# Kernel optimization log

Measured on AMD Instinct MI355X. Metric: run time of the kernel, lower is better.

## Reference

```python
import jax, jax.numpy as jnp
import numpy as np

B, IN, H, OUT = 1024, 512, 1024, 512   # tokens, input, hidden (MoE width), output
E, K, LAYERS = 8, 2, 10                 # experts, top-k, repeated MoE applications
EPS = 1e-10
LOSS_COEF = 0.01


def setup_inputs() -> dict:
    key = jax.random.key(0)
    ks = jax.random.split(key, 8)
    s = 0.02  # small init scale for weights
    return {
        "x": jax.random.normal(ks[0], (B, IN), jnp.float32),
        "enc_w": jax.random.normal(ks[1], (IN, H), jnp.float32) * s,
        "enc_b": jnp.zeros((H,), jnp.float32),
        "w_gate": jax.random.normal(ks[2], (H, E), jnp.float32) * s,
        "w1": jax.random.normal(ks[3], (E, H, H), jnp.float32) * s,
        "b1": jnp.zeros((E, H), jnp.float32),
        "w2": jax.random.normal(ks[4], (E, H, H), jnp.float32) * s,
        "b2": jnp.zeros((E, H), jnp.float32),
        "dec_w": jax.random.normal(ks[5], (H, OUT), jnp.float32) * s,
        "dec_b": jnp.zeros((OUT,), jnp.float32),
    }


def _cv_squared(v):
    # torch .var() is unbiased (ddof=1)
    return jnp.var(v, ddof=1) / (jnp.mean(v) ** 2 + EPS)


def _moe_layer(h, w_gate, w1, b1, w2, b2):
    # top-k gating (eval / no-noise path of noisy_top_k_gating)
    logits = h @ w_gate                                  # [B, E]
    top_vals, top_idx = jax.lax.top_k(logits, K)         # [B, K]
    gk = jax.nn.softmax(top_vals, axis=-1)               # softmax over top-k logits
    b = h.shape[0]
    gates = jnp.zeros((b, E), h.dtype).at[jnp.arange(b)[:, None], top_idx].set(gk)
    importance = gates.sum(axis=0)                       # [E]
    load = (gates > 0).sum(axis=0).astype(h.dtype)       # [E]
    aux = LOSS_COEF * (_cv_squared(importance) + _cv_squared(load))
    # experts: Linear -> ReLU -> Linear; combine weighted by gates
    # (dense-over-experts form; math identical to sparse dispatch/combine)
    hid = jax.nn.relu(jnp.einsum('bh,ehf->bef', h, w1) + b1)  # [B, E, H]
    y = jnp.einsum('bef,efo->beo', hid, w2) + b2              # [B, E, H]
    out = jnp.einsum('be,beo->bo', gates, y)                  # [B, H]
    return out, aux


def reference(x, enc_w, enc_b, w_gate, w1, b1, w2, b2, dec_w, dec_b):
    h = jax.nn.relu(x @ enc_w + enc_b)
    loss = jnp.zeros((), h.dtype)
    for _ in range(LAYERS):  # same MoE module (shared params) applied 10 times
        h, aux = _moe_layer(h, w_gate, w1, b1, w2, b2)
        loss = loss + aux
    out = jax.nn.relu(h @ dec_w + dec_b)
    return out, loss
```

## Files before the change

kernel.cpp:

```cpp
#include <hip/hip_runtime.h>
#include <math.h>

#define TPB 256
#define GTPB 512
typedef unsigned short u16;
typedef unsigned int u32;
typedef __bf16 bf16x8 __attribute__((ext_vector_type(8)));
typedef float f32x4 __attribute__((ext_vector_type(4)));

namespace {
constexpr int NTOK  = 1024;
constexpr int IND   = 512;
constexpr int HD    = 1024;
constexpr int OUTD  = 512;
constexpr int NE    = 8;
constexpr int NSLOT = 2048;
}

__device__ __forceinline__ u16 f2bf(float f) {
  u32 x = __float_as_uint(f);
  x += 0x7fffu + ((x >> 16) & 1u);
  return (u16)(x >> 16);
}
__device__ __forceinline__ float bf2f(u16 u) { return __uint_as_float(((u32)u) << 16); }
__device__ __forceinline__ void split2(float v, u16& h, u16& l) {
  h = f2bf(v);
  l = f2bf(v - bf2f(h));
}

__device__ __forceinline__ void gll16(const void* g, void* l) {
  __builtin_amdgcn_global_load_lds((const __attribute__((address_space(1))) void*)g,
                                   (__attribute__((address_space(3))) void*)l, 16, 0, 0);
}


__global__ __launch_bounds__(TPB)
void transpose_split(const float* __restrict__ in, u16* __restrict__ ohi,
                     u16* __restrict__ olo, int K, int N)
{
  const int z = blockIdx.z;
  in  += (size_t)z * K * N;
  ohi += (size_t)z * K * N;
  olo += (size_t)z * K * N;
  __shared__ float tile[32][33];
  const int k0 = blockIdx.y * 32, n0 = blockIdx.x * 32;
  const int tx = threadIdx.x & 31, ty = threadIdx.x >> 5;
#pragma unroll
  for (int i = 0; i < 4; ++i) {
    int k = ty + i * 8;
    tile[k][tx] = in[(size_t)(k0 + k) * N + n0 + tx];
  }
  __syncthreads();
#pragma unroll
  for (int i = 0; i < 4; ++i) {
    int n = ty + i * 8;
    float v = tile[tx][n];
    u16 h, l; split2(v, h, l);
    int kk = k0 + tx, nn = n0 + n;
    size_t o = ((size_t)((nn >> 7) * (K >> 6) + (kk >> 6)) << 13)
             + (((nn & 127) * 8 + (((kk >> 3) & 7) ^ (nn & 7))) << 3) + (kk & 7);
    ohi[o] = h; olo[o] = l;
  }
}

__global__ __launch_bounds__(TPB)
void split_rows(const float* __restrict__ in, u16* __restrict__ oh,
                u16* __restrict__ ol, int nelem)
{
  int i = blockIdx.x * TPB + threadIdx.x;
  if (i * 4 >= nelem) return;
  float4 v = ((const float4*)in)[i];
  ushort4 H, L;
  split2(v.x, H.x, L.x); split2(v.y, H.y, L.y);
  split2(v.z, H.z, L.z); split2(v.w, H.w, L.w);
  ((ushort4*)oh)[i] = H;
  ((ushort4*)ol)[i] = L;
}

template<bool RELU, bool GROUPED, bool GATHER, bool SPLIT_OUT>
__global__ __launch_bounds__(GTPB)
void gemm_split(const u16* __restrict__ Ah, const u16* __restrict__ Al,
                const int* __restrict__ gatherIdx,
                const u16* __restrict__ Bh, const u16* __restrict__ Bl,
                const float* __restrict__ bias,
                float* __restrict__ Cf, u16* __restrict__ Ch, u16* __restrict__ Cl,
                const int* __restrict__ seg_off, const int* __restrict__ seg_cnt,
                int M, int K, int N)
{
  const int e = GROUPED ? blockIdx.z : 0;
  int cnt = M, base = 0;
  if (GROUPED) { cnt = seg_cnt[e]; base = seg_off[e]; }
  const int tm = blockIdx.y, tn = blockIdx.x;
  if (tm * 64 >= cnt) return;

  __shared__ u16 smem[73728];
  constexpr int AHo = 0, ALo = 4096, BHo = 8192, BLo = 16384, BUF = 24576;

  const int t = threadIdx.x;
  const int wid = t >> 6, lane = t & 63;
  const int wr = wid >> 2, wc = wid & 3;

  const u16* aph; const u16* apl;
  {
    int row = t >> 3, kblk = t & 7;
    int kbs = kblk ^ (row & 7);
    int row_in = tm * 64 + row;
    int rv = row_in < cnt ? row_in : 0;
    int src;
    if (GATHER)      src = gatherIdx[base + rv];
    else             src = GROUPED ? base + rv : rv;
    size_t off = (size_t)src * K + kbs * 8;
    aph = Ah + off; apl = Al + off;
  }
  const u16* bsh; const u16* bsl;
  {
    size_t pb = ((size_t)((GROUPED ? e : 0) * (N >> 7) + tn) * (K >> 6)) << 13;
    bsh = Bh + pb; bsl = Bl + pb;
  }

  auto stage = [&](int bb, int ks) {
    gll16(aph + (ks << 6), &smem[bb + AHo + t * 8]);
    gll16(apl + (ks << 6), &smem[bb + ALo + t * 8]);
    const size_t tb = (size_t)ks << 13;
#pragma unroll
    for (int i = 0; i < 2; ++i) {
      int so = (t + i * GTPB) * 8;
      gll16(bsh + tb + so, &smem[bb + BHo + so]);
      gll16(bsl + tb + so, &smem[bb + BLo + so]);
    }
  };

  f32x4 acc[2][2];
#pragma unroll
  for (int i = 0; i < 2; ++i)
#pragma unroll
    for (int j = 0; j < 2; ++j) acc[i][j] = (f32x4){0.f, 0.f, 0.f, 0.f};

  auto compute = [&](int bb) {
#pragma unroll
    for (int s = 0; s < 2; ++s) {
      const int kb = s * 4 + (lane >> 4);
      bf16x8 fah[2], fal[2];
#pragma unroll
      for (int fr = 0; fr < 2; ++fr) {
        int ar = wr * 32 + fr * 16 + (lane & 15);
        int off = bb + ar * 64 + ((kb ^ (ar & 7)) << 3);
        fah[fr] = *(const bf16x8*)&smem[AHo + off];
        fal[fr] = *(const bf16x8*)&smem[ALo + off];
      }
      bf16x8 fbh[2], fbl[2];
#pragma unroll
      for (int fc = 0; fc < 2; ++fc) {
        int bn = wc * 32 + fc * 16 + (lane & 15);
        int off = bb + bn * 64 + ((kb ^ (bn & 7)) << 3);
        fbh[fc] = *(const bf16x8*)&smem[BHo + off];
        fbl[fc] = *(const bf16x8*)&smem[BLo + off];
      }
      __builtin_amdgcn_s_setprio(1);
#pragma unroll
      for (int fr = 0; fr < 2; ++fr)
#pragma unroll
        for (int fc = 0; fc < 2; ++fc) {
          acc[fr][fc] = __builtin_amdgcn_mfma_f32_16x16x32_bf16(fah[fr], fbh[fc], acc[fr][fc], 0, 0, 0);
          acc[fr][fc] = __builtin_amdgcn_mfma_f32_16x16x32_bf16(fah[fr], fbl[fc], acc[fr][fc], 0, 0, 0);
          acc[fr][fc] = __builtin_amdgcn_mfma_f32_16x16x32_bf16(fal[fr], fbh[fc], acc[fr][fc], 0, 0, 0);
        }
      __builtin_amdgcn_s_setprio(0);
    }
  };

  const int NT = K >> 6;
  stage(0, 0);
  stage(BUF, 1);
  for (int tt = 0; tt < NT; ++tt) {
    if (tt == NT - 1) { asm volatile("s_waitcnt vmcnt(0)" ::: "memory"); }
    else              { asm volatile("s_waitcnt vmcnt(6)" ::: "memory"); }
    __builtin_amdgcn_s_barrier();
    asm volatile("" ::: "memory");
    if (tt + 2 < NT) stage(((tt + 2) % 3) * BUF, tt + 2);
    compute((tt % 3) * BUF);
    asm volatile("" ::: "memory");
  }

  const float* bp = bias + (GROUPED ? (size_t)e * N : 0);
#pragma unroll
  for (int fr = 0; fr < 2; ++fr) {
#pragma unroll
    for (int q = 0; q < 4; ++q) {
      int row_in = tm * 64 + wr * 32 + fr * 16 + ((lane >> 4) << 2) + q;
      if (row_in >= cnt) continue;
      size_t orow = (size_t)(GROUPED ? base + row_in : row_in);
#pragma unroll
      for (int fc = 0; fc < 2; ++fc) {
        int col = tn * 128 + wc * 32 + fc * 16 + (lane & 15);
        float v = acc[fr][fc][q] + bp[col];
        if (RELU) v = fmaxf(v, 0.f);
        if (SPLIT_OUT) {
          u16 h, l; split2(v, h, l);
          Ch[orow * N + col] = h;
          Cl[orow * N + col] = l;
        } else {
          Cf[orow * N + col] = v;
        }
      }
    }
  }
}

__global__ __launch_bounds__(TPB)
void gate_split(const u16* __restrict__ hh, const u16* __restrict__ hl,
                const float* __restrict__ w_gate,
                int* __restrict__ eidx, float* __restrict__ gval)
{
  const int b = blockIdx.x, t = threadIdx.x;
  ushort4 H = ((const ushort4*)(hh + (size_t)b * HD))[t];
  ushort4 L = ((const ushort4*)(hl + (size_t)b * HD))[t];
  float hv[4] = { bf2f(H.x) + bf2f(L.x), bf2f(H.y) + bf2f(L.y),
                  bf2f(H.z) + bf2f(L.z), bf2f(H.w) + bf2f(L.w) };
  float acc[NE] = {};
  const int i0 = t * 4;
#pragma unroll
  for (int j = 0; j < 4; ++j) {
    const float4* wg = (const float4*)(w_gate + (size_t)(i0 + j) * NE);
    float4 w0 = wg[0], w1 = wg[1];
    acc[0] = fmaf(hv[j], w0.x, acc[0]); acc[1] = fmaf(hv[j], w0.y, acc[1]);
    acc[2] = fmaf(hv[j], w0.z, acc[2]); acc[3] = fmaf(hv[j], w0.w, acc[3]);
    acc[4] = fmaf(hv[j], w1.x, acc[4]); acc[5] = fmaf(hv[j], w1.y, acc[5]);
    acc[6] = fmaf(hv[j], w1.z, acc[6]); acc[7] = fmaf(hv[j], w1.w, acc[7]);
  }
  __shared__ float red[TPB][NE];
#pragma unroll
  for (int e = 0; e < NE; ++e) red[t][e] = acc[e];
  __syncthreads();
  for (int s = TPB / 2; s > 0; s >>= 1) {
    if (t < s) {
#pragma unroll
      for (int e = 0; e < NE; ++e) red[t][e] += red[t + s][e];
    }
    __syncthreads();
  }
  if (t == 0) {
    float v1 = -1e30f; int e1 = 0;
#pragma unroll
    for (int e = 0; e < NE; ++e) { float v = red[0][e]; if (v > v1) { v1 = v; e1 = e; } }
    float v2 = -1e30f; int e2 = 0;
#pragma unroll
    for (int e = 0; e < NE; ++e) {
      if (e == e1) continue;
      float v = red[0][e]; if (v > v2) { v2 = v; e2 = e; }
    }
    float ev = expf(v2 - v1);
    eidx[b * 2] = e1;  eidx[b * 2 + 1] = e2;
    gval[b * 2] = 1.f / (1.f + ev);  gval[b * 2 + 1] = ev / (1.f + ev);
  }
}

__global__ __launch_bounds__(TPB)
void stats_scatter(const int* __restrict__ eidx, const float* __restrict__ gval,
                   float* __restrict__ loss, int* __restrict__ seg_off,
                   int* __restrict__ seg_cnt, int* __restrict__ slot_token,
                   int* __restrict__ slot_of)
{
  const int t = threadIdx.x;
  float imp[NE] = {};
  int   cnt[NE] = {};
  for (int s = t; s < NSLOT; s += TPB) {
    int e = eidx[s]; float g = gval[s];
#pragma unroll
    for (int q = 0; q < NE; ++q) if (q == e) { imp[q] += g; cnt[q]++; }
  }
  __shared__ float rimp[TPB][NE];
  __shared__ int   rcnt[TPB][NE];
#pragma unroll
  for (int e = 0; e < NE; ++e) { rimp[t][e] = imp[e]; rcnt[t][e] = cnt[e]; }
  __syncthreads();
  for (int s = TPB / 2; s > 0; s >>= 1) {
    if (t < s) {
#pragma unroll
      for (int e = 0; e < NE; ++e) { rimp[t][e] += rimp[t + s][e]; rcnt[t][e] += rcnt[t + s][e]; }
    }
    __syncthreads();
  }
  __shared__ int s_off[NE], s_fill[NE];
  if (t == 0) {
    float mi = 0.f, ml = 0.f;
#pragma unroll
    for (int e = 0; e < NE; ++e) { mi += rimp[0][e]; ml += (float)rcnt[0][e]; }
    mi /= NE; ml /= NE;
    float vi = 0.f, vl = 0.f;
#pragma unroll
    for (int e = 0; e < NE; ++e) {
      float di = rimp[0][e] - mi; vi += di * di;
      float dl = (float)rcnt[0][e] - ml; vl += dl * dl;
    }
    vi /= (NE - 1); vl /= (NE - 1);
    loss[0] += 0.01f * (vi / (mi * mi + 1e-10f) + vl / (ml * ml + 1e-10f));
    int off = 0;
#pragma unroll
    for (int e = 0; e < NE; ++e) {
      seg_off[e] = off; seg_cnt[e] = rcnt[0][e];
      s_off[e] = off; s_fill[e] = 0; off += rcnt[0][e];
    }
  }
  __syncthreads();
  for (int s = t; s < NSLOT; s += TPB) {
    int e = eidx[s];
    int pos = s_off[e] + atomicAdd(&s_fill[e], 1);
    slot_token[pos] = s >> 1;
    slot_of[s] = pos;
  }
}

template<bool GATE>
__global__ __launch_bounds__(TPB)
void combine_gate(const float* __restrict__ y, const float* __restrict__ gv_in,
                  const int* __restrict__ slot_of, const float* __restrict__ w_gate,
                  u16* __restrict__ hh, u16* __restrict__ hl,
                  int* __restrict__ eidx, float* __restrict__ gval)
{
  const int b = blockIdx.x, t = threadIdx.x;
  const int p0 = slot_of[b * 2], p1 = slot_of[b * 2 + 1];
  const float g0 = gv_in[b * 2], g1 = gv_in[b * 2 + 1];
  float4 a = ((const float4*)(y + (size_t)p0 * HD))[t];
  float4 c = ((const float4*)(y + (size_t)p1 * HD))[t];
  float v[4] = { g0 * a.x + g1 * c.x, g0 * a.y + g1 * c.y,
                 g0 * a.z + g1 * c.z, g0 * a.w + g1 * c.w };
  ushort4 H, L;
  split2(v[0], H.x, L.x); split2(v[1], H.y, L.y);
  split2(v[2], H.z, L.z); split2(v[3], H.w, L.w);
  ((ushort4*)(hh + (size_t)b * HD))[t] = H;
  ((ushort4*)(hl + (size_t)b * HD))[t] = L;

  if (GATE) {
    float acc[NE] = {};
    const int i0 = t * 4;
#pragma unroll
    for (int j = 0; j < 4; ++j) {
      const float4* wg = (const float4*)(w_gate + (size_t)(i0 + j) * NE);
      float4 w0 = wg[0], w1 = wg[1];
      acc[0] = fmaf(v[j], w0.x, acc[0]); acc[1] = fmaf(v[j], w0.y, acc[1]);
      acc[2] = fmaf(v[j], w0.z, acc[2]); acc[3] = fmaf(v[j], w0.w, acc[3]);
      acc[4] = fmaf(v[j], w1.x, acc[4]); acc[5] = fmaf(v[j], w1.y, acc[5]);
      acc[6] = fmaf(v[j], w1.z, acc[6]); acc[7] = fmaf(v[j], w1.w, acc[7]);
    }
    __shared__ float red[TPB][NE];
#pragma unroll
    for (int e = 0; e < NE; ++e) red[t][e] = acc[e];
    __syncthreads();
    for (int s = TPB / 2; s > 0; s >>= 1) {
      if (t < s) {
#pragma unroll
        for (int e = 0; e < NE; ++e) red[t][e] += red[t + s][e];
      }
      __syncthreads();
    }
    if (t == 0) {
      float v1 = -1e30f; int e1 = 0;
#pragma unroll
      for (int e = 0; e < NE; ++e) { float vv = red[0][e]; if (vv > v1) { v1 = vv; e1 = e; } }
      float v2 = -1e30f; int e2 = 0;
#pragma unroll
      for (int e = 0; e < NE; ++e) {
        if (e == e1) continue;
        float vv = red[0][e]; if (vv > v2) { v2 = vv; e2 = e; }
      }
      float ev = expf(v2 - v1);
      eidx[b * 2] = e1;  eidx[b * 2 + 1] = e2;
      gval[b * 2] = 1.f / (1.f + ev);  gval[b * 2 + 1] = ev / (1.f + ev);
    }
  }
}

__global__ void init_kernel(float* loss) { loss[0] = 0.f; }
__global__ void write_loss(const float* __restrict__ loss, float* __restrict__ out)
{ out[0] = loss[0]; }

template<bool RELU, bool GROUPED, bool GATHER>
__global__ __launch_bounds__(TPB)
void gemm_f32(const float* __restrict__ A, const int* __restrict__ gatherIdx,
              const float* __restrict__ B, const float* __restrict__ bias,
              float* __restrict__ C, const int* __restrict__ seg_off,
              const int* __restrict__ seg_cnt, int M, int K, int N)
{
  const int e = GROUPED ? blockIdx.z : 0;
  int cnt = M, base = 0;
  if (GROUPED) { cnt = seg_cnt[e]; base = seg_off[e]; }
  const int tm = blockIdx.y, tn = blockIdx.x;
  if (tm * 64 >= cnt) return;
  const float* Bp = B + (size_t)e * K * N;
  const float* bp = bias + (size_t)e * N;
  __shared__ float As[16][68];
  __shared__ float Bs[16][64];
  const int t = threadIdx.x;
  const int rm0 = (t >> 4) << 2, cn0 = (t & 15) << 2;
  int arow[4]; bool aval[4];
#pragma unroll
  for (int i = 0; i < 4; ++i) {
    int idx = t + i * TPB;
    int r = idx >> 4;
    int row_in = tm * 64 + r;
    bool v = row_in < cnt;
    int src;
    if (GATHER) src = v ? gatherIdx[base + row_in] : 0;
    else        src = v ? (GROUPED ? base + row_in : row_in) : 0;
    arow[i] = src; aval[i] = v;
  }
  float acc[4][4] = {};
  for (int k0 = 0; k0 < K; k0 += 16) {
#pragma unroll
    for (int i = 0; i < 4; ++i) {
      int idx = t + i * TPB;
      int r = idx >> 4, kk = idx & 15;
      As[kk][r] = aval[i] ? A[(size_t)arow[i] * K + k0 + kk] : 0.f;
    }
#pragma unroll
    for (int i = 0; i < 4; ++i) {
      int idx = t + i * TPB;
      int kk = idx >> 6, n = idx & 63;
      Bs[kk][n] = Bp[(size_t)(k0 + kk) * N + tn * 64 + n];
    }
    __syncthreads();
#pragma unroll
    for (int kk = 0; kk < 16; ++kk) {
      const float4 a4 = *(const float4*)&As[kk][rm0];
      const float4 b4 = *(const float4*)&Bs[kk][cn0];
      float av[4] = {a4.x, a4.y, a4.z, a4.w};
      float bv[4] = {b4.x, b4.y, b4.z, b4.w};
#pragma unroll
      for (int i = 0; i < 4; ++i)
#pragma unroll
        for (int j = 0; j < 4; ++j) acc[i][j] = fmaf(av[i], bv[j], acc[i][j]);
    }
    __syncthreads();
  }
#pragma unroll
  for (int i = 0; i < 4; ++i) {
    int row_in = tm * 64 + rm0 + i;
    if (row_in >= cnt) continue;
    size_t orow = (size_t)(base + row_in);
    float v0 = acc[i][0] + bp[tn * 64 + cn0 + 0];
    float v1 = acc[i][1] + bp[tn * 64 + cn0 + 1];
    float v2 = acc[i][2] + bp[tn * 64 + cn0 + 2];
    float v3 = acc[i][3] + bp[tn * 64 + cn0 + 3];
    if (RELU) { v0 = fmaxf(v0, 0.f); v1 = fmaxf(v1, 0.f); v2 = fmaxf(v2, 0.f); v3 = fmaxf(v3, 0.f); }
    *(float4*)&C[orow * N + tn * 64 + cn0] = make_float4(v0, v1, v2, v3);
  }
}

__global__ __launch_bounds__(TPB)
void gate_f32(const float* __restrict__ h, const float* __restrict__ w_gate,
              int* __restrict__ eidx, float* __restrict__ gval)
{
  const int b = blockIdx.x, t = threadIdx.x;
  float acc[NE] = {};
  const float* hb = h + (size_t)b * HD;
  for (int i = t; i < HD; i += TPB) {
    float hv = hb[i];
    const float* wg = w_gate + (size_t)i * NE;
#pragma unroll
    for (int e = 0; e < NE; ++e) acc[e] = fmaf(hv, wg[e], acc[e]);
  }
  __shared__ float red[TPB][NE];
#pragma unroll
  for (int e = 0; e < NE; ++e) red[t][e] = acc[e];
  __syncthreads();
  for (int s = TPB / 2; s > 0; s >>= 1) {
    if (t < s) {
#pragma unroll
      for (int e = 0; e < NE; ++e) red[t][e] += red[t + s][e];
    }
    __syncthreads();
  }
  if (t == 0) {
    float v1 = -1e30f; int e1 = 0;
#pragma unroll
    for (int e = 0; e < NE; ++e) { float v = red[0][e]; if (v > v1) { v1 = v; e1 = e; } }
    float v2 = -1e30f; int e2 = 0;
#pragma unroll
    for (int e = 0; e < NE; ++e) {
      if (e == e1) continue;
      float v = red[0][e]; if (v > v2) { v2 = v; e2 = e; }
    }
    float ev = expf(v2 - v1);
    eidx[b * 2] = e1;  eidx[b * 2 + 1] = e2;
    gval[b * 2] = 1.f / (1.f + ev);  gval[b * 2 + 1] = ev / (1.f + ev);
  }
}

__global__ __launch_bounds__(TPB)
void combine_f32(const float* __restrict__ y, const float* __restrict__ gval,
                 const int* __restrict__ slot_of, float* __restrict__ h)
{
  const int b = blockIdx.x, t = threadIdx.x;
  const int p0 = slot_of[b * 2], p1 = slot_of[b * 2 + 1];
  const float g0 = gval[b * 2], g1 = gval[b * 2 + 1];
  const float4* y0 = (const float4*)(y + (size_t)p0 * HD);
  const float4* y1 = (const float4*)(y + (size_t)p1 * HD);
  float4* hb = (float4*)(h + (size_t)b * HD);
  for (int i = t; i < HD / 4; i += TPB) {
    float4 a = y0[i], c = y1[i];
    hb[i] = make_float4(g0 * a.x + g1 * c.x, g0 * a.y + g1 * c.y,
                        g0 * a.z + g1 * c.z, g0 * a.w + g1 * c.w);
  }
}


extern "C" void kernel_launch(void* const* d_in, const int* in_sizes, int n_in,
                              void* d_out, int out_size, void* d_ws, size_t ws_size,
                              hipStream_t stream)
{
  const float* x      = (const float*)d_in[0];
  const float* enc_w  = (const float*)d_in[1];
  const float* enc_b  = (const float*)d_in[2];
  const float* w_gate = (const float*)d_in[3];
  const float* w1     = (const float*)d_in[4];
  const float* b1     = (const float*)d_in[5];
  const float* w2     = (const float*)d_in[6];
  const float* b2     = (const float*)d_in[7];
  const float* dec_w  = (const float*)d_in[8];
  const float* dec_b  = (const float*)d_in[9];
  float* outp = (float*)d_out;
  dim3 blk(TPB);
  dim3 gblk(GTPB);

  const size_t NEED = 100ull << 20;
  if (ws_size >= NEED) {
    char* p = (char*)d_ws;
    auto alloc = [&](size_t bytes) { char* r = p; p += (bytes + 255) & ~(size_t)255; return r; };
    u16* w1t_h = (u16*)alloc((size_t)NE * HD * HD * 2);
    u16* w1t_l = (u16*)alloc((size_t)NE * HD * HD * 2);
    u16* w2t_h = (u16*)alloc((size_t)NE * HD * HD * 2);
    u16* w2t_l = (u16*)alloc((size_t)NE * HD * HD * 2);
    u16* ewt_h = (u16*)alloc((size_t)IND * HD * 2);
    u16* ewt_l = (u16*)alloc((size_t)IND * HD * 2);
    u16* dwt_h = (u16*)alloc((size_t)HD * OUTD * 2);
    u16* dwt_l = (u16*)alloc((size_t)HD * OUTD * 2);
    u16* x_h   = (u16*)alloc((size_t)NTOK * IND * 2);
    u16* x_l   = (u16*)alloc((size_t)NTOK * IND * 2);
    u16* h_h   = (u16*)alloc((size_t)NTOK * HD * 2);
    u16* h_l   = (u16*)alloc((size_t)NTOK * HD * 2);
    u16* hid_h = (u16*)alloc((size_t)NSLOT * HD * 2);
    u16* hid_l = (u16*)alloc((size_t)NSLOT * HD * 2);
    float* y   = (float*)alloc((size_t)NSLOT * HD * 4);
    int*   eidx       = (int*)alloc(NSLOT * 4);
    float* gval       = (float*)alloc(NSLOT * 4);
    int*   slot_of    = (int*)alloc(NSLOT * 4);
    int*   slot_token = (int*)alloc(NSLOT * 4);
    int*   seg_off    = (int*)alloc(256);
    int*   seg_cnt    = (int*)alloc(256);
    float* loss       = (float*)alloc(256);

    init_kernel<<<1, 1, 0, stream>>>(loss);
    transpose_split<<<dim3(HD / 32, HD / 32, NE), blk, 0, stream>>>(w1, w1t_h, w1t_l, HD, HD);
    transpose_split<<<dim3(HD / 32, HD / 32, NE), blk, 0, stream>>>(w2, w2t_h, w2t_l, HD, HD);
    transpose_split<<<dim3(HD / 32, IND / 32, 1), blk, 0, stream>>>(enc_w, ewt_h, ewt_l, IND, HD);
    transpose_split<<<dim3(OUTD / 32, HD / 32, 1), blk, 0, stream>>>(dec_w, dwt_h, dwt_l, HD, OUTD);
    split_rows<<<(NTOK * IND / 4 + TPB - 1) / TPB, blk, 0, stream>>>(x, x_h, x_l, NTOK * IND);

    gemm_split<true, false, false, true><<<dim3(HD / 128, NTOK / 64, 1), gblk, 0, stream>>>(
        x_h, x_l, nullptr, ewt_h, ewt_l, enc_b, nullptr, h_h, h_l, nullptr, nullptr,
        NTOK, IND, HD);

    gate_split<<<NTOK, blk, 0, stream>>>(h_h, h_l, w_gate, eidx, gval);
    for (int L = 0; L < 10; ++L) {
      stats_scatter<<<1, blk, 0, stream>>>(eidx, gval, loss, seg_off, seg_cnt,
                                           slot_token, slot_of);
      gemm_split<true, true, true, true><<<dim3(HD / 128, NSLOT / 64, NE), gblk, 0, stream>>>(
          h_h, h_l, slot_token, w1t_h, w1t_l, b1, nullptr, hid_h, hid_l,
          seg_off, seg_cnt, 0, HD, HD);
      gemm_split<false, true, false, false><<<dim3(HD / 128, NSLOT / 64, NE), gblk, 0, stream>>>(
          hid_h, hid_l, nullptr, w2t_h, w2t_l, b2, y, nullptr, nullptr,
          seg_off, seg_cnt, 0, HD, HD);
      if (L < 9)
        combine_gate<true><<<NTOK, blk, 0, stream>>>(y, gval, slot_of, w_gate,
                                                     h_h, h_l, eidx, gval);
      else
        combine_gate<false><<<NTOK, blk, 0, stream>>>(y, gval, slot_of, w_gate,
                                                      h_h, h_l, eidx, gval);
    }

    gemm_split<true, false, false, false><<<dim3(OUTD / 128, NTOK / 64, 1), gblk, 0, stream>>>(
        h_h, h_l, nullptr, dwt_h, dwt_l, dec_b, outp, nullptr, nullptr, nullptr, nullptr,
        NTOK, HD, OUTD);
    write_loss<<<1, 1, 0, stream>>>(loss, outp + NTOK * OUTD);
    return;
  }

  char* ws = (char*)d_ws;
  float* h   = (float*)(ws);
  float* hid = (float*)(ws + (4u  << 20));
  float* y   = (float*)(ws + (12u << 20));
  char* sp = ws + (20u << 20);
  int*   eidx       = (int*)sp;    sp += NSLOT * 4;
  float* gval       = (float*)sp;  sp += NSLOT * 4;
  int*   slot_of    = (int*)sp;    sp += NSLOT * 4;
  int*   slot_token = (int*)sp;    sp += NSLOT * 4;
  int*   seg_off    = (int*)sp;    sp += 64;
  int*   seg_cnt    = (int*)sp;    sp += 64;
  float* loss       = (float*)sp;  sp += 64;

  init_kernel<<<1, 1, 0, stream>>>(loss);
  gemm_f32<true, false, false><<<dim3(HD / 64, NTOK / 64, 1), blk, 0, stream>>>(
      x, nullptr, enc_w, enc_b, h, nullptr, nullptr, NTOK, IND, HD);
  for (int L = 0; L < 10; ++L) {
    gate_f32<<<NTOK, blk, 0, stream>>>(h, w_gate, eidx, gval);
    stats_scatter<<<1, blk, 0, stream>>>(eidx, gval, loss, seg_off, seg_cnt,
                                         slot_token, slot_of);
    gemm_f32<true, true, true><<<dim3(HD / 64, NTOK / 64, NE), blk, 0, stream>>>(
        h, slot_token, w1, b1, hid, seg_off, seg_cnt, 0, HD, HD);
    gemm_f32<false, true, false><<<dim3(HD / 64, NTOK / 64, NE), blk, 0, stream>>>(
        hid, nullptr, w2, b2, y, seg_off, seg_cnt, 0, HD, HD);
    combine_f32<<<NTOK, blk, 0, stream>>>(y, gval, slot_of, h);
  }
  gemm_f32<true, false, false><<<dim3(OUTD / 64, NTOK / 64, 1), blk, 0, stream>>>(
      h, nullptr, dec_w, dec_b, outp, nullptr, nullptr, NTOK, HD, OUTD);
  write_loss<<<1, 1, 0, stream>>>(loss, outp + NTOK * OUTD);
}
```

Baseline: 874.7 us.

## Shrink GEMM tiles to 64x64 with 256 threads and double buffering

The split-bf16 GEMM tile goes from 64x128 with 512 threads and a triple-buffered hand-waited pipeline to 64x64 with 256 threads and a simple double buffer synchronized by __syncthreads. The weight pre-layout is changed to match 64-column panels. The aim is more blocks and higher occupancy (LDS drops from 144KB to 64KB per block) for the unevenly sized expert segments. In exchange, each block reuses less data and the weaker pipeline exposes more memory latency.

```diff
diff --git a/kernel.cpp b/kernel.cpp
--- a/kernel.cpp
+++ b/kernel.cpp
@@ -2,7 +2,6 @@
 #include <math.h>
 
 #define TPB 256
-#define GTPB 512
 typedef unsigned short u16;
 typedef unsigned int u32;
 typedef __bf16 bf16x8 __attribute__((ext_vector_type(8)));
@@ -57,8 +56,8 @@
     float v = tile[tx][n];
     u16 h, l; split2(v, h, l);
     int kk = k0 + tx, nn = n0 + n;
-    size_t o = ((size_t)((nn >> 7) * (K >> 6) + (kk >> 6)) << 13)
-             + (((nn & 127) * 8 + (((kk >> 3) & 7) ^ (nn & 7))) << 3) + (kk & 7);
+    size_t o = ((size_t)((nn >> 6) * (K >> 6) + (kk >> 6)) << 12)
+             + (((nn & 63) * 8 + (((kk >> 3) & 7) ^ (nn & 7))) << 3) + (kk & 7);
     ohi[o] = h; olo[o] = l;
   }
 }
@@ -78,7 +77,7 @@
 }
 
 template<bool RELU, bool GROUPED, bool GATHER, bool SPLIT_OUT>
-__global__ __launch_bounds__(GTPB)
+__global__ __launch_bounds__(TPB)
 void gemm_split(const u16* __restrict__ Ah, const u16* __restrict__ Al,
                 const int* __restrict__ gatherIdx,
                 const u16* __restrict__ Bh, const u16* __restrict__ Bl,
@@ -93,16 +92,18 @@
   const int tm = blockIdx.y, tn = blockIdx.x;
   if (tm * 64 >= cnt) return;
 
-  __shared__ u16 smem[73728];
-  constexpr int AHo = 0, ALo = 4096, BHo = 8192, BLo = 16384, BUF = 24576;
+  __shared__ u16 smem[32768];
+  constexpr int AHo = 0, ALo = 4096, BHo = 8192, BLo = 12288, BUF = 16384;
 
   const int t = threadIdx.x;
   const int wid = t >> 6, lane = t & 63;
-  const int wr = wid >> 2, wc = wid & 3;
-
-  const u16* aph; const u16* apl;
-  {
-    int row = t >> 3, kblk = t & 7;
+  const int wr = wid >> 1, wc = wid & 1;
+
+  const u16* aph[2]; const u16* apl[2];
+#pragma unroll
+  for (int i = 0; i < 2; ++i) {
+    int slot = t + i * TPB;
+    int row = slot >> 3, kblk = slot & 7;
     int kbs = kblk ^ (row & 7);
     int row_in = tm * 64 + row;
     int rv = row_in < cnt ? row_in : 0;
@@ -110,21 +111,25 @@
     if (GATHER)      src = gatherIdx[base + rv];
     else             src = GROUPED ? base + rv : rv;
     size_t off = (size_t)src * K + kbs * 8;
-    aph = Ah + off; apl = Al + off;
+    aph[i] = Ah + off; apl[i] = Al + off;
   }
   const u16* bsh; const u16* bsl;
   {
-    size_t pb = ((size_t)((GROUPED ? e : 0) * (N >> 7) + tn) * (K >> 6)) << 13;
+    size_t pb = ((size_t)((GROUPED ? e : 0) * (N >> 6) + tn) * (K >> 6)) << 12;
     bsh = Bh + pb; bsl = Bl + pb;
   }
 
   auto stage = [&](int bb, int ks) {
-    gll16(aph + (ks << 6), &smem[bb + AHo + t * 8]);
-    gll16(apl + (ks << 6), &smem[bb + ALo + t * 8]);
-    const size_t tb = (size_t)ks << 13;
 #pragma unroll
     for (int i = 0; i < 2; ++i) {
-      int so = (t + i * GTPB) * 8;
+      int so = (t + i * TPB) * 8;
+      gll16(aph[i] + (ks << 6), &smem[bb + AHo + so]);
+      gll16(apl[i] + (ks << 6), &smem[bb + ALo + so]);
+    }
+    const size_t tb = (size_t)ks << 12;
+#pragma unroll
+    for (int i = 0; i < 2; ++i) {
+      int so = (t + i * TPB) * 8;
       gll16(bsh + tb + so, &smem[bb + BHo + so]);
       gll16(bsl + tb + so, &smem[bb + BLo + so]);
     }
@@ -170,16 +175,13 @@
   };
 
   const int NT = K >> 6;
+  int buf = 0;
   stage(0, 0);
-  stage(BUF, 1);
   for (int tt = 0; tt < NT; ++tt) {
-    if (tt == NT - 1) { asm volatile("s_waitcnt vmcnt(0)" ::: "memory"); }
-    else              { asm volatile("s_waitcnt vmcnt(6)" ::: "memory"); }
-    __builtin_amdgcn_s_barrier();
-    asm volatile("" ::: "memory");
-    if (tt + 2 < NT) stage(((tt + 2) % 3) * BUF, tt + 2);
-    compute((tt % 3) * BUF);
-    asm volatile("" ::: "memory");
+    __syncthreads();
+    if (tt + 1 < NT) stage((buf ^ 1) * BUF, tt + 1);
+    compute(buf * BUF);
+    buf ^= 1;
   }
 
   const float* bp = bias + (GROUPED ? (size_t)e * N : 0);
@@ -192,7 +194,7 @@
       size_t orow = (size_t)(GROUPED ? base + row_in : row_in);
 #pragma unroll
       for (int fc = 0; fc < 2; ++fc) {
-        int col = tn * 128 + wc * 32 + fc * 16 + (lane & 15);
+        int col = tn * 64 + wc * 32 + fc * 16 + (lane & 15);
         float v = acc[fr][fc][q] + bp[col];
         if (RELU) v = fmaxf(v, 0.f);
         if (SPLIT_OUT) {
@@ -521,7 +523,6 @@
   const float* dec_b  = (const float*)d_in[9];
   float* outp = (float*)d_out;
   dim3 blk(TPB);
-  dim3 gblk(GTPB);
 
   const size_t NEED = 100ull << 20;
   if (ws_size >= NEED) {
@@ -557,7 +558,7 @@
     transpose_split<<<dim3(OUTD / 32, HD / 32, 1), blk, 0, stream>>>(dec_w, dwt_h, dwt_l, HD, OUTD);
     split_rows<<<(NTOK * IND / 4 + TPB - 1) / TPB, blk, 0, stream>>>(x, x_h, x_l, NTOK * IND);
 
-    gemm_split<true, false, false, true><<<dim3(HD / 128, NTOK / 64, 1), gblk, 0, stream>>>(
+    gemm_split<true, false, false, true><<<dim3(HD / 64, NTOK / 64, 1), blk, 0, stream>>>(
         x_h, x_l, nullptr, ewt_h, ewt_l, enc_b, nullptr, h_h, h_l, nullptr, nullptr,
         NTOK, IND, HD);
 
@@ -565,10 +566,10 @@
     for (int L = 0; L < 10; ++L) {
       stats_scatter<<<1, blk, 0, stream>>>(eidx, gval, loss, seg_off, seg_cnt,
                                            slot_token, slot_of);
-      gemm_split<true, true, true, true><<<dim3(HD / 128, NSLOT / 64, NE), gblk, 0, stream>>>(
+      gemm_split<true, true, true, true><<<dim3(HD / 64, NSLOT / 64, NE), blk, 0, stream>>>(
           h_h, h_l, slot_token, w1t_h, w1t_l, b1, nullptr, hid_h, hid_l,
           seg_off, seg_cnt, 0, HD, HD);
-      gemm_split<false, true, false, false><<<dim3(HD / 128, NSLOT / 64, NE), gblk, 0, stream>>>(
+      gemm_split<false, true, false, false><<<dim3(HD / 64, NSLOT / 64, NE), blk, 0, stream>>>(
           hid_h, hid_l, nullptr, w2t_h, w2t_l, b2, y, nullptr, nullptr,
           seg_off, seg_cnt, 0, HD, HD);
       if (L < 9)
@@ -579,7 +580,7 @@
                                                       h_h, h_l, eidx, gval);
     }
 
-    gemm_split<true, false, false, false><<<dim3(OUTD / 128, NTOK / 64, 1), gblk, 0, stream>>>(
+    gemm_split<true, false, false, false><<<dim3(OUTD / 64, NTOK / 64, 1), blk, 0, stream>>>(
         h_h, h_l, nullptr, dwt_h, dwt_l, dec_b, outp, nullptr, nullptr, nullptr, nullptr,
         NTOK, HD, OUTD);
     write_loss<<<1, 1, 0, stream>>>(loss, outp + NTOK * OUTD);
```

Result: faster. 775.8 us (-11.3%).
